# Performance work log

Measured on AMD Instinct MI355X. Metric: run time of the kernel, lower is better.

The kernel has to match this reference:

```python
import jax, jax.numpy as jnp
import numpy as np

B, T, C = 2, 4096, 512
H = 8
MEMORY = 256  # window: key j visible to query i iff 0 <= i - j <= MEMORY


def setup_inputs() -> dict:
    key = jax.random.key(0)
    k1, k2, k3 = jax.random.split(key, 3)
    x = jax.random.normal(k1, (B, T, C), dtype=jnp.float32)
    w_attn = jax.random.normal(k2, (3 * C, C), dtype=jnp.float32) * 0.02
    w_proj = jax.random.normal(k3, (C, C), dtype=jnp.float32) * 0.02
    return {"x": x, "w_attn": w_attn, "w_proj": w_proj}


def reference(x, w_attn, w_proj):
    b, t, c = x.shape
    d = c // H
    # fused QKV projection (Linear without bias): x @ W^T
    qkv = jnp.einsum('btc,fc->btf', x, w_attn)  # [B,T,3C]
    q, k, v = jnp.split(qkv, 3, axis=-1)
    # [B,T,C] -> [B,H,T,d]
    q = q.reshape(b, t, H, d).transpose(0, 2, 1, 3)
    k = k.reshape(b, t, H, d).transpose(0, 2, 1, 3)
    v = v.reshape(b, t, H, d).transpose(0, 2, 1, 3)
    # sliding-window causal mask: tril(0) & ~tril(-memory-1)
    i = jnp.arange(t)[:, None]
    j = jnp.arange(t)[None, :]
    mask = (j <= i) & (i - j <= MEMORY)  # [T,T] bool
    scores = jnp.einsum('bhqd,bhkd->bhqk', q, k) * (1.0 / np.sqrt(d))
    scores = jnp.where(mask, scores, -jnp.inf)
    attn = jax.nn.softmax(scores, axis=-1)
    y = jnp.einsum('bhqk,bhkd->bhqd', attn, v)  # [B,H,T,d]
    y = y.transpose(0, 2, 1, 3).reshape(b, t, c)
    # output projection
    y = jnp.einsum('btc,fc->btf', y, w_proj)
    return y
```

## Files before the change

### kernel.cpp

```cpp
#include <hip/hip_runtime.h>
#include <hip/hip_bf16.h>
#include <stdint.h>

#define BB 2
#define TT 4096
#define CC 512
#define HH 8
#define MEM 256

typedef unsigned short u16;
typedef __bf16 bf16x8 __attribute__((ext_vector_type(8)));
typedef float floatx4 __attribute__((ext_vector_type(4)));

__device__ inline u16 f2bf(float f) {
  uint32_t u = __float_as_uint(f);
  uint32_t r = (u + 0x7fffu + ((u >> 16) & 1u)) >> 16;
  return (u16)r;
}
__device__ inline u16 f2bf_r(float f) {
  return (u16)((__float_as_uint(f) + 0x8000u) >> 16);
}

__device__ inline void gld16(const u16* g, u16* lds) {
  __builtin_amdgcn_global_load_lds(
      (const __attribute__((address_space(1))) uint32_t*)g,
      (__attribute__((address_space(3))) uint32_t*)lds, 16, 0, 0);
}

#define BARM() asm volatile("" ::: "memory")

__global__ __launch_bounds__(256) void cvt_all(const float* __restrict__ x,
                                               const float* __restrict__ wa,
                                               const float* __restrict__ wp,
                                               u16* __restrict__ xb,
                                               u16* __restrict__ wab,
                                               u16* __restrict__ wpb) {
  int i = blockIdx.x * 256 + threadIdx.x;
  const float* s; u16* d; int off;
  if (i < 1048576) { s = x; d = xb; off = i; }
  else if (i < 1245184) { s = wa; d = wab; off = i - 1048576; }
  else { s = wp; d = wpb; off = i - 1245184; }
  float4 v = *reinterpret_cast<const float4*>(s + (size_t)off * 4);
  ushort4 o;
  o.x = f2bf(v.x); o.y = f2bf(v.y); o.z = f2bf(v.z); o.w = f2bf(v.w);
  *reinterpret_cast<ushort4*>(d + (size_t)off * 4) = o;
}

__device__ inline void stage_hA(const u16* __restrict__ G, u16* lds, int K,
                                int gr0, int koff, int half, int wv, int lane) {
#pragma unroll
  for (int j = 0; j < 2; j++) {
    int lrow = (j * 8 + wv) * 8 + (lane >> 3);
    int row = (lrow & 63) + ((lrow >> 6) << 7) + (half << 6);
    int blk = (lane & 7) ^ (row & 7);
    gld16(G + (size_t)(gr0 + row) * K + koff + blk * 8,
          lds + (size_t)row * 64 + (lane & 7) * 8);
  }
}
__device__ inline void stage_hB(const u16* __restrict__ G, u16* lds, int K,
                                int gr0, int koff, int half, int wv, int lane) {
#pragma unroll
  for (int j = 0; j < 2; j++) {
    int lrow = (j * 8 + wv) * 8 + (lane >> 3);
    int row = (lrow & 31) + ((lrow >> 5) << 6) + (half << 5);
    int blk = (lane & 7) ^ (row & 7);
    gld16(G + (size_t)(gr0 + row) * K + koff + blk * 8,
          lds + (size_t)row * 64 + (lane & 7) * 8);
  }
}

#define PHASE(MQ, NQ, STAGE, WAITV)                                            \
  {                                                                            \
    bf16x8 af[4][2], bfv[2][2];                                                \
    _Pragma("unroll") for (int fm = 0; fm < 4; fm++) {                         \
      int row = wm * 128 + MQ * 64 + fm * 16 + l16;                            \
      const u16* p = Ad + (size_t)row * 64;                                    \
      af[fm][0] = *(const bf16x8*)(p + ((quad ^ (row & 7)) << 3));             \
      af[fm][1] = *(const bf16x8*)(p + (((4 + quad) ^ (row & 7)) << 3));       \
    }                                                                          \
    _Pragma("unroll") for (int fn = 0; fn < 2; fn++) {                         \
      int row = wn * 64 + NQ * 32 + fn * 16 + l16;                             \
      const u16* p = Bd + (size_t)row * 64;                                    \
      bfv[fn][0] = *(const bf16x8*)(p + ((quad ^ (row & 7)) << 3));            \
      bfv[fn][1] = *(const bf16x8*)(p + (((4 + quad) ^ (row & 7)) << 3));      \
    }                                                                          \
    STAGE;                                                                     \
    BARM();                                                                    \
    __builtin_amdgcn_s_barrier();                                              \
    asm volatile("s_waitcnt lgkmcnt(0)" ::: "memory");                         \
    __builtin_amdgcn_sched_barrier(0);                                         \
    __builtin_amdgcn_s_setprio(1);                                             \
    _Pragma("unroll") for (int fm = 0; fm < 4; fm++)                           \
      _Pragma("unroll") for (int fn = 0; fn < 2; fn++) {                       \
        acc[MQ * 4 + fm][NQ * 2 + fn] =                                        \
            __builtin_amdgcn_mfma_f32_16x16x32_bf16(                           \
                af[fm][0], bfv[fn][0], acc[MQ * 4 + fm][NQ * 2 + fn], 0, 0, 0);\
        acc[MQ * 4 + fm][NQ * 2 + fn] =                                        \
            __builtin_amdgcn_mfma_f32_16x16x32_bf16(                           \
                af[fm][1], bfv[fn][1], acc[MQ * 4 + fm][NQ * 2 + fn], 0, 0, 0);\
      }                                                                        \
    __builtin_amdgcn_s_setprio(0);                                             \
    WAITV;                                                                     \
    BARM();                                                                    \
    __builtin_amdgcn_s_barrier();                                              \
    BARM();                                                                    \
  }

__global__ __launch_bounds__(512, 2) void gemm256(const u16* __restrict__ A,
                                                  const u16* __restrict__ Bw,
                                                  u16* __restrict__ C,
                                                  int M, int N, int K) {
  __shared__ __align__(16) u16 As[2][256 * 64];
  __shared__ __align__(16) u16 Bs[2][256 * 64];
  const int tid = threadIdx.x;
  const int lane = tid & 63, wv = tid >> 6;
  const int quad = lane >> 4, l16 = lane & 15;
  const int wm = wv >> 2, wn = wv & 3;

  const int nbx = N >> 8;
  const int nwg = (M >> 8) * nbx;
  int wg = blockIdx.x;
  if ((nwg & 7) == 0) wg = (wg & 7) * (nwg >> 3) + (wg >> 3);
  const int m0 = (wg / nbx) << 8, n0 = (wg % nbx) << 8;

  const int nK = K >> 6;
  floatx4 acc[8][4] = {};

  stage_hA(A, As[0], K, m0, 0, 0, wv, lane);
  stage_hA(A, As[0], K, m0, 0, 1, wv, lane);
  stage_hB(Bw, Bs[0], K, n0, 0, 0, wv, lane);
  stage_hB(Bw, Bs[0], K, n0, 0, 1, wv, lane);
  if (nK > 1) {
    stage_hA(A, As[1], K, m0, 64, 0, wv, lane);
    stage_hB(Bw, Bs[1], K, n0, 64, 0, wv, lane);
    asm volatile("s_waitcnt vmcnt(4)" ::: "memory");
  } else {
    asm volatile("s_waitcnt vmcnt(0)" ::: "memory");
  }
  BARM();
  __builtin_amdgcn_s_barrier();
  BARM();

  for (int t = 0; t < nK; ++t) {
    const int d = t & 1;
    u16* Ad = As[d]; u16* Bd = Bs[d];
    u16* An = As[d ^ 1]; u16* Bn = Bs[d ^ 1];
    const int k1 = (t + 1) << 6, k2 = (t + 2) << 6;

    PHASE(0, 0, { if (t + 1 < nK) stage_hA(A, An, K, m0, k1, 1, wv, lane); }, {})
    PHASE(0, 1, { if (t + 1 < nK) stage_hB(Bw, Bn, K, n0, k1, 1, wv, lane); }, {})
    PHASE(1, 0, { if (t + 2 < nK) stage_hA(A, Ad, K, m0, k2, 0, wv, lane); }, {})
    PHASE(1, 1, { if (t + 2 < nK) stage_hB(Bw, Bd, K, n0, k2, 0, wv, lane); },
          { if (t + 2 < nK) asm volatile("s_waitcnt vmcnt(4)" ::: "memory");
            else            asm volatile("s_waitcnt vmcnt(0)" ::: "memory"); })
  }

#pragma unroll
  for (int mi = 0; mi < 8; mi++) {
    int row = m0 + wm * 128 + mi * 16 + quad * 4;
#pragma unroll
    for (int ni = 0; ni < 4; ni++) {
      int col = n0 + wn * 64 + ni * 16 + l16;
#pragma unroll
      for (int r = 0; r < 4; r++)
        C[(size_t)(row + r) * N + col] = f2bf(acc[mi][ni][r]);
    }
  }
}

__global__ __launch_bounds__(256) void gemm_bt_n64(const u16* __restrict__ A,
                                                   const u16* __restrict__ Bw,
                                                   float* __restrict__ C,
                                                   int M, int N, int K) {
  __shared__ __align__(16) u16 As[128 * 32];
  __shared__ __align__(16) u16 Bs[64 * 32];
  const int tid = threadIdx.x;
  const int w = tid >> 6, lane = tid & 63, quad = lane >> 4, l16 = lane & 15;
  const int m0 = blockIdx.x * 128, n0 = blockIdx.y * 64;

  floatx4 acc[2][4] = {};
  const int nK = K >> 5;
  for (int kb = 0; kb < nK; ++kb) {
    const int kof = kb * 32;
    {
      int c = tid;
      gld16(A + (size_t)(m0 + (c >> 2)) * K + kof + (c & 3) * 8, As + (size_t)c * 8);
      c = tid + 256;
      gld16(A + (size_t)(m0 + (c >> 2)) * K + kof + (c & 3) * 8, As + (size_t)c * 8);
      c = tid;
      gld16(Bw + (size_t)(n0 + (c >> 2)) * K + kof + (c & 3) * 8, Bs + (size_t)c * 8);
    }
    __syncthreads();
    bf16x8 af[2], bfr[4];
#pragma unroll
    for (int i = 0; i < 2; i++)
      af[i] = *reinterpret_cast<const bf16x8*>(&As[(w * 32 + i * 16 + l16) * 32 + quad * 8]);
#pragma unroll
    for (int i = 0; i < 4; i++)
      bfr[i] = *reinterpret_cast<const bf16x8*>(&Bs[(i * 16 + l16) * 32 + quad * 8]);
#pragma unroll
    for (int mi = 0; mi < 2; mi++)
#pragma unroll
      for (int ni = 0; ni < 4; ni++)
        acc[mi][ni] = __builtin_amdgcn_mfma_f32_16x16x32_bf16(af[mi], bfr[ni], acc[mi][ni], 0, 0, 0);
    __syncthreads();
  }
#pragma unroll
  for (int mi = 0; mi < 2; mi++) {
    int row = m0 + w * 32 + mi * 16 + quad * 4;
#pragma unroll
    for (int ni = 0; ni < 4; ni++) {
      int col = n0 + ni * 16 + l16;
#pragma unroll
      for (int r = 0; r < 4; r++)
        C[(size_t)(row + r) * N + col] = acc[mi][ni][r];
    }
  }
}

__global__ __launch_bounds__(256, 2) void attn_win(const u16* __restrict__ qkv,
                                                   u16* __restrict__ y) {
  const int q0 = blockIdx.x * 128;
  const int h = blockIdx.y;
  const int b = blockIdx.z;
  const int tid = threadIdx.x;
  const int w = tid >> 6, lane = tid & 63, quad = lane >> 4, l16 = lane & 15;

  __shared__ __align__(16) u16 Qs[128 * 64];
  __shared__ __align__(16) u16 Ks[64 * 64];
  __shared__ __align__(16) u16 Vt[64 * 72];
  __shared__ __align__(16) u16 Ps[4][32 * 72];

  const size_t baseQ = ((size_t)(b * TT + q0)) * 1536 + h * 64;
#pragma unroll
  for (int j = 0; j < 4; j++) {
    int c = tid + j * 256, row = c >> 3, blk = (c & 7) ^ (row & 7);
    gld16(qkv + baseQ + (size_t)row * 1536 + blk * 8, Qs + (size_t)c * 8);
  }
  __syncthreads();
  bf16x8 qf[2][2];
#pragma unroll
  for (int mi = 0; mi < 2; mi++) {
    int row = w * 32 + mi * 16 + l16;
    qf[mi][0] = *reinterpret_cast<const bf16x8*>(&Qs[row * 64 + (quad ^ (l16 & 7)) * 8]);
    qf[mi][1] = *reinterpret_cast<const bf16x8*>(&Qs[row * 64 + ((quad + 4) ^ (l16 & 7)) * 8]);
#pragma unroll
    for (int e = 0; e < 8; e++) {
      qf[mi][0][e] = qf[mi][0][e] * (__bf16)0.125f;
      qf[mi][1][e] = qf[mi][1][e] * (__bf16)0.125f;
    }
  }

  floatx4 acc_o[2][4] = {};
  float l_acc[2][4] = {{0.f, 0.f, 0.f, 0.f}, {0.f, 0.f, 0.f, 0.f}};

  const int s_min = (q0 >= 256) ? 0 : ((256 - q0) >> 6);
  const int key_v = tid >> 3, dc_v = tid & 7;
  const int key_v1 = (tid + 256) >> 3, dc_v1 = tid & 7;

  uint4 vp0, vp1;
  {
    size_t baseV = ((size_t)(b * TT + (q0 - 256 + s_min * 64))) * 1536 + 1024 + h * 64;
    vp0 = *reinterpret_cast<const uint4*>(qkv + baseV + (size_t)key_v * 1536 + dc_v * 8);
    vp1 = *reinterpret_cast<const uint4*>(qkv + baseV + (size_t)key_v1 * 1536 + dc_v1 * 8);
  }

  for (int s = s_min; s < 6; ++s) {
    const int k0 = q0 - 256 + s * 64;
    const size_t baseK = ((size_t)(b * TT + k0)) * 1536 + 512 + h * 64;
    {
      int c = tid, row = c >> 3, blk = (c & 7) ^ (row & 7);
      gld16(qkv + baseK + (size_t)row * 1536 + blk * 8, Ks + (size_t)c * 8);
      c = tid + 256; row = c >> 3; blk = (c & 7) ^ (row & 7);
      gld16(qkv + baseK + (size_t)row * 1536 + blk * 8, Ks + (size_t)c * 8);
    }
    {
      u16 tmp[8];
      *reinterpret_cast<uint4*>(tmp) = vp0;
      int col = key_v ^ (dc_v * 8);
#pragma unroll
      for (int e = 0; e < 8; e++) Vt[(dc_v * 8 + e) * 72 + col] = tmp[e];
      *reinterpret_cast<uint4*>(tmp) = vp1;
      col = key_v1 ^ (dc_v1 * 8);
#pragma unroll
      for (int e = 0; e < 8; e++) Vt[(dc_v1 * 8 + e) * 72 + col] = tmp[e];
    }
    if (s < 5) {
      size_t baseV = ((size_t)(b * TT + k0 + 64)) * 1536 + 1024 + h * 64;
      vp0 = *reinterpret_cast<const uint4*>(qkv + baseV + (size_t)key_v * 1536 + dc_v * 8);
      vp1 = *reinterpret_cast<const uint4*>(qkv + baseV + (size_t)key_v1 * 1536 + dc_v1 * 8);
    }
    __syncthreads();

    int mode = 0;
    if (s == 0) mode = (w < 2) ? 1 : 3;
    else if (s == 1) mode = (w < 2) ? 0 : 1;
    else if (s == 4) mode = (w < 2) ? 2 : 0;
    else if (s == 5) mode = (w < 2) ? 3 : 2;

    if (mode != 3) {
      bf16x8 bfr[4][2];
#pragma unroll
      for (int nt = 0; nt < 4; nt++) {
        int krow = nt * 16 + l16;
        bfr[nt][0] = *reinterpret_cast<const bf16x8*>(&Ks[krow * 64 + (quad ^ (l16 & 7)) * 8]);
        bfr[nt][1] = *reinterpret_cast<const bf16x8*>(&Ks[krow * 64 + ((quad + 4) ^ (l16 & 7)) * 8]);
      }
      floatx4 sc[2][4] = {};
#pragma unroll
      for (int mi = 0; mi < 2; mi++)
#pragma unroll
        for (int nt = 0; nt < 4; nt++) {
          sc[mi][nt] = __builtin_amdgcn_mfma_f32_16x16x32_bf16(qf[mi][0], bfr[nt][0], sc[mi][nt], 0, 0, 0);
          sc[mi][nt] = __builtin_amdgcn_mfma_f32_16x16x32_bf16(qf[mi][1], bfr[nt][1], sc[mi][nt], 0, 0, 0);
        }
      const int hqb = (w & 1) * 32 + quad * 4;
      if (mode == 1) {
#pragma unroll
        for (int mi = 0; mi < 2; mi++)
#pragma unroll
          for (int nt = 0; nt < 4; nt++)
#pragma unroll
            for (int r = 0; r < 4; r++)
              if (hqb + mi * 16 + r > nt * 16 + l16) sc[mi][nt][r] = -1e30f;
      } else if (mode == 2) {
#pragma unroll
        for (int mi = 0; mi < 2; mi++)
#pragma unroll
          for (int nt = 0; nt < 4; nt++)
#pragma unroll
            for (int r = 0; r < 4; r++)
              if (hqb + mi * 16 + r < nt * 16 + l16) sc[mi][nt][r] = -1e30f;
      }
#pragma unroll
      for (int mi = 0; mi < 2; mi++)
#pragma unroll
        for (int nt = 0; nt < 4; nt++)
#pragma unroll
          for (int r = 0; r < 4; r++) {
            float p = __expf(sc[mi][nt][r] - 4.0f);
            l_acc[mi][r] += p;
            Ps[w][(mi * 16 + quad * 4 + r) * 72 + nt * 16 + l16] = f2bf_r(p);
          }
#pragma unroll
      for (int mi = 0; mi < 2; mi++)
#pragma unroll
        for (int ki = 0; ki < 2; ki++) {
          bf16x8 pf = *reinterpret_cast<const bf16x8*>(
              &Ps[w][(mi * 16 + l16) * 72 + ki * 32 + quad * 8]);
#pragma unroll
          for (int nt = 0; nt < 4; nt++) {
            int d = nt * 16 + l16;
            bf16x8 vf = *reinterpret_cast<const bf16x8*>(
                &Vt[d * 72 + ((ki * 32 + quad * 8) ^ (d & 56))]);
            acc_o[mi][nt] = __builtin_amdgcn_mfma_f32_16x16x32_bf16(pf, vf, acc_o[mi][nt], 0, 0, 0);
          }
        }
    }
    __syncthreads();
  }
#pragma unroll
  for (int mi = 0; mi < 2; mi++)
#pragma unroll
    for (int r = 0; r < 4; r++) {
      float l = l_acc[mi][r];
      l += __shfl_xor(l, 1);
      l += __shfl_xor(l, 2);
      l += __shfl_xor(l, 4);
      l += __shfl_xor(l, 8);
      float inv = 1.f / l;
      int row = q0 + w * 32 + mi * 16 + quad * 4 + r;
      size_t base = (size_t)(b * TT + row) * 512 + h * 64;
#pragma unroll
      for (int nt = 0; nt < 4; nt++)
        y[base + nt * 16 + l16] = f2bf(acc_o[mi][nt][r] * inv);
    }
}

extern "C" void kernel_launch(void* const* d_in, const int* in_sizes, int n_in,
                              void* d_out, int out_size, void* d_ws, size_t ws_size,
                              hipStream_t stream) {
  const float* x = (const float*)d_in[0];
  const float* w_attn = (const float*)d_in[1];
  const float* w_proj = (const float*)d_in[2];
  float* out = (float*)d_out;

  u16* xb = (u16*)d_ws;
  u16* wab = xb + (size_t)8192 * 512;
  u16* wpb = wab + (size_t)1536 * 512;
  u16* qkv = wpb + (size_t)512 * 512;
  u16* yb = qkv + (size_t)8192 * 1536;

  cvt_all<<<5120, 256, 0, stream>>>(x, w_attn, w_proj, xb, wab, wpb);
  gemm256<<<192, 512, 0, stream>>>(xb, wab, qkv, 8192, 1536, 512);
  attn_win<<<dim3(TT / 128, HH, BB), 256, 0, stream>>>(qkv, yb);
  gemm_bt_n64<<<dim3(64, 8), 256, 0, stream>>>(yb, wpb, out, 8192, 512, 512);
}
```

Measured before the change: 128.4 us.

## Shrink QKV GEMM N-tile to 192 to fill all CUs with 256 workgroups

The QKV projection GEMM now uses a 256x192 output tile instead of 256x256. With N=1536 this raises the grid from 192 to 256 workgroups, which matches the 256 CUs and avoids leaving part of the GPU idle. The B-tile staging is redone so the two halves load 128 and 64 rows. Each wave now covers 48 columns, and the second N phase issues one MFMA column fragment instead of two. The trade-off is less operand reuse per tile and uneven work between the two N phases.

Result: no change. 126.6 us (-1.4%).

```diff
diff --git a/kernel.cpp b/kernel.cpp
--- a/kernel.cpp
+++ b/kernel.cpp
@@ -59,27 +59,35 @@
 }
 __device__ inline void stage_hB(const u16* __restrict__ G, u16* lds, int K,
                                 int gr0, int koff, int half, int wv, int lane) {
-#pragma unroll
-  for (int j = 0; j < 2; j++) {
-    int lrow = (j * 8 + wv) * 8 + (lane >> 3);
-    int row = (lrow & 31) + ((lrow >> 5) << 6) + (half << 5);
+  if (half == 0) {
+#pragma unroll
+    for (int j = 0; j < 2; j++) {
+      int lrow = (j * 8 + wv) * 8 + (lane >> 3);
+      int row = (lrow & 31) + (lrow >> 5) * 48;
+      int blk = (lane & 7) ^ (row & 7);
+      gld16(G + (size_t)(gr0 + row) * K + koff + blk * 8,
+            lds + (size_t)row * 64 + (lane & 7) * 8);
+    }
+  } else {
+    int lrow = wv * 8 + (lane >> 3);
+    int row = 32 + (lrow & 15) + (lrow >> 4) * 48;
     int blk = (lane & 7) ^ (row & 7);
     gld16(G + (size_t)(gr0 + row) * K + koff + blk * 8,
           lds + (size_t)row * 64 + (lane & 7) * 8);
   }
 }
 
-#define PHASE(MQ, NQ, STAGE, WAITV)                                            \
+#define PHASE(MQ, NQ, NF, STAGE, WAITV)                                        \
   {                                                                            \
-    bf16x8 af[4][2], bfv[2][2];                                                \
+    bf16x8 af[4][2], bfv[NF][2];                                               \
     _Pragma("unroll") for (int fm = 0; fm < 4; fm++) {                         \
       int row = wm * 128 + MQ * 64 + fm * 16 + l16;                            \
       const u16* p = Ad + (size_t)row * 64;                                    \
       af[fm][0] = *(const bf16x8*)(p + ((quad ^ (row & 7)) << 3));             \
       af[fm][1] = *(const bf16x8*)(p + (((4 + quad) ^ (row & 7)) << 3));       \
     }                                                                          \
-    _Pragma("unroll") for (int fn = 0; fn < 2; fn++) {                         \
-      int row = wn * 64 + NQ * 32 + fn * 16 + l16;                             \
+    _Pragma("unroll") for (int fn = 0; fn < NF; fn++) {                        \
+      int row = wn * 48 + NQ * 32 + fn * 16 + l16;                             \
       const u16* p = Bd + (size_t)row * 64;                                    \
       bfv[fn][0] = *(const bf16x8*)(p + ((quad ^ (row & 7)) << 3));            \
       bfv[fn][1] = *(const bf16x8*)(p + (((4 + quad) ^ (row & 7)) << 3));      \
@@ -91,7 +99,7 @@
     __builtin_amdgcn_sched_barrier(0);                                         \
     __builtin_amdgcn_s_setprio(1);                                             \
     _Pragma("unroll") for (int fm = 0; fm < 4; fm++)                           \
-      _Pragma("unroll") for (int fn = 0; fn < 2; fn++) {                       \
+      _Pragma("unroll") for (int fn = 0; fn < NF; fn++) {                      \
         acc[MQ * 4 + fm][NQ * 2 + fn] =                                        \
             __builtin_amdgcn_mfma_f32_16x16x32_bf16(                           \
                 af[fm][0], bfv[fn][0], acc[MQ * 4 + fm][NQ * 2 + fn], 0, 0, 0);\
@@ -111,20 +119,20 @@
                                                   u16* __restrict__ C,
                                                   int M, int N, int K) {
   __shared__ __align__(16) u16 As[2][256 * 64];
-  __shared__ __align__(16) u16 Bs[2][256 * 64];
+  __shared__ __align__(16) u16 Bs[2][192 * 64];
   const int tid = threadIdx.x;
   const int lane = tid & 63, wv = tid >> 6;
   const int quad = lane >> 4, l16 = lane & 15;
   const int wm = wv >> 2, wn = wv & 3;
 
-  const int nbx = N >> 8;
+  const int nbx = N / 192;
   const int nwg = (M >> 8) * nbx;
   int wg = blockIdx.x;
   if ((nwg & 7) == 0) wg = (wg & 7) * (nwg >> 3) + (wg >> 3);
-  const int m0 = (wg / nbx) << 8, n0 = (wg % nbx) << 8;
+  const int m0 = (wg / nbx) << 8, n0 = (wg % nbx) * 192;
 
   const int nK = K >> 6;
-  floatx4 acc[8][4] = {};
+  floatx4 acc[8][3] = {};
 
   stage_hA(A, As[0], K, m0, 0, 0, wv, lane);
   stage_hA(A, As[0], K, m0, 0, 1, wv, lane);
@@ -147,10 +155,10 @@
     u16* An = As[d ^ 1]; u16* Bn = Bs[d ^ 1];
     const int k1 = (t + 1) << 6, k2 = (t + 2) << 6;
 
-    PHASE(0, 0, { if (t + 1 < nK) stage_hA(A, An, K, m0, k1, 1, wv, lane); }, {})
-    PHASE(0, 1, { if (t + 1 < nK) stage_hB(Bw, Bn, K, n0, k1, 1, wv, lane); }, {})
-    PHASE(1, 0, { if (t + 2 < nK) stage_hA(A, Ad, K, m0, k2, 0, wv, lane); }, {})
-    PHASE(1, 1, { if (t + 2 < nK) stage_hB(Bw, Bd, K, n0, k2, 0, wv, lane); },
+    PHASE(0, 0, 2, { if (t + 1 < nK) stage_hA(A, An, K, m0, k1, 1, wv, lane); }, {})
+    PHASE(0, 1, 1, { if (t + 1 < nK) stage_hB(Bw, Bn, K, n0, k1, 1, wv, lane); }, {})
+    PHASE(1, 0, 2, { if (t + 2 < nK) stage_hA(A, Ad, K, m0, k2, 0, wv, lane); }, {})
+    PHASE(1, 1, 1, { if (t + 2 < nK) stage_hB(Bw, Bd, K, n0, k2, 0, wv, lane); },
           { if (t + 2 < nK) asm volatile("s_waitcnt vmcnt(4)" ::: "memory");
             else            asm volatile("s_waitcnt vmcnt(0)" ::: "memory"); })
   }
@@ -159,8 +167,8 @@
   for (int mi = 0; mi < 8; mi++) {
     int row = m0 + wm * 128 + mi * 16 + quad * 4;
 #pragma unroll
-    for (int ni = 0; ni < 4; ni++) {
-      int col = n0 + wn * 64 + ni * 16 + l16;
+    for (int ni = 0; ni < 3; ni++) {
+      int col = n0 + wn * 48 + ni * 16 + l16;
 #pragma unroll
       for (int r = 0; r < 4; r++)
         C[(size_t)(row + r) * N + col] = f2bf(acc[mi][ni][r]);
@@ -392,7 +400,7 @@
   u16* yb = qkv + (size_t)8192 * 1536;
 
   cvt_all<<<5120, 256, 0, stream>>>(x, w_attn, w_proj, xb, wab, wpb);
-  gemm256<<<192, 512, 0, stream>>>(xb, wab, qkv, 8192, 1536, 512);
+  gemm256<<<256, 512, 0, stream>>>(xb, wab, qkv, 8192, 1536, 512);
   attn_win<<<dim3(TT / 128, HH, BB), 256, 0, stream>>>(qkv, yb);
   gemm_bt_n64<<<dim3(64, 8), 256, 0, stream>>>(yb, wpb, out, 8192, 512, 512);
 }
```
